# Kernel tuning notes

Hardware: AMD Instinct MI355X
Metric: run time of the kernel (lower is better)

## Reference

```python
import jax, jax.numpy as jnp
import numpy as np

V, E, H, LE, B, T = 32001, 512, 512, 512, 128, 512
EPS = 1e-5


def setup_inputs() -> dict:
    key = jax.random.key(0)
    ks = jax.random.split(key, 12)
    s = 0.02
    return {
        "label": jax.random.randint(ks[0], (B, T), 0, V, dtype=jnp.int64) if jax.config.jax_enable_x64 else jax.random.randint(ks[0], (B, T), 0, V, dtype=jnp.int32),
        "label_len": jax.random.randint(ks[1], (B,), 0, T, dtype=jnp.int32),
        "embed_w": jax.random.normal(ks[2], (V, E), jnp.float32) * s,
        "i2h_w": jax.random.normal(ks[3], (5 * H, E), jnp.float32) * s,
        "i2h_b": jax.random.normal(ks[4], (5 * H,), jnp.float32) * s,
        "h2h_w": jax.random.normal(ks[5], (5 * H, H), jnp.float32) * s,
        "h2h_b": jax.random.normal(ks[6], (5 * H,), jnp.float32) * s,
        "lin0_w": jax.random.normal(ks[7], (LE, H), jnp.float32) * s,
        "lin0_b": jax.random.normal(ks[8], (LE,), jnp.float32) * s,
        "bn0_g": jnp.ones((LE,), jnp.float32),
        "bn0_b": jnp.zeros((LE,), jnp.float32),
        "lin1_w": jax.random.normal(ks[9], (LE, LE), jnp.float32) * s,
        "lin1_b": jax.random.normal(ks[10], (LE,), jnp.float32) * s,
        "bn1_g": jnp.ones((LE,), jnp.float32),
        "bn1_b": jnp.zeros((LE,), jnp.float32),
    }


def _batchnorm(x, g, b):
    # BatchNorm1d in training mode: biased batch statistics over batch dim
    m = jnp.mean(x, axis=0)
    v = jnp.mean((x - m) ** 2, axis=0)
    return (x - m) * jax.lax.rsqrt(v + EPS) * g + b


def reference(label, label_len, embed_w, i2h_w, i2h_b, h2h_w, h2h_b,
              lin0_w, lin0_b, bn0_g, bn0_b, lin1_w, lin1_b, bn1_g, bn1_b):
    xt = embed_w[label]                                   # [B,T,E]
    pre = jnp.einsum('bte,ge->btg', xt, i2h_w) + i2h_b    # precomputed i2h, [B,T,5H]
    pre = pre.transpose(1, 0, 2)                          # [T,B,5H]

    def step(carry, p_t):
        h, c = carry
        s = p_t + h @ h2h_w.T + h2h_b                     # [B,5H]
        sig = jax.nn.sigmoid(s[:, :3 * H])
        in_g, f_g, out_g = sig[:, :H], sig[:, H:2 * H], sig[:, 2 * H:3 * H]
        in_t = jnp.maximum(s[:, 3 * H:4 * H], s[:, 4 * H:5 * H])  # maxout transform
        nc = f_g * c + in_g * in_t
        nh = out_g * jnp.tanh(nc)
        return (nh, nc), nh

    h0 = jnp.zeros((B, H), pre.dtype)
    _, outs = jax.lax.scan(step, (h0, h0), pre)           # outs: [T,B,H]

    # pick output at timestep label_len[i] for each sample
    x = outs[label_len, jnp.arange(B)]                    # [B,H]

    x = _batchnorm(x @ lin0_w.T + lin0_b, bn0_g, bn0_b)
    x = jax.nn.relu(x)                                    # dropout identity (eval)
    x = _batchnorm(x @ lin1_w.T + lin1_b, bn1_g, bn1_b)
    return x
```

## Files before the change

### kernel.cpp

```cpp
#include <hip/hip_runtime.h>

typedef _Float16 h16x8 __attribute__((ext_vector_type(8)));
typedef _Float16 h16x4 __attribute__((ext_vector_type(4)));
typedef float fx4 __attribute__((ext_vector_type(4)));
typedef unsigned int u32x4 __attribute__((ext_vector_type(4)));
typedef unsigned long long ull;

#define PRE_S 2560.0f
#define PRE_INV (1.0f / 2560.0f)

__global__ __launch_bounds__(256) void f2h_kernel(const float* __restrict__ src,
                                                  _Float16* __restrict__ dst,
                                                  int n4) {
  int i = blockIdx.x * 256 + threadIdx.x;
  if (i < n4) {
    float4 v = ((const float4*)src)[i];
    h16x4 o = {(_Float16)v.x, (_Float16)v.y, (_Float16)v.z, (_Float16)v.w};
    *(h16x4*)&dst[i * 4] = o;
  }
}

__global__ __launch_bounds__(256) void gemm1_kernel(
    const int* __restrict__ label, const int* __restrict__ label_len,
    const float* __restrict__ embed_w,
    const _Float16* __restrict__ Bh,
    signed char* __restrict__ pre8) {
  const int bx = blockIdx.x;
  const int by = blockIdx.y;
  const int bidx = by >> 2;
  const int t0 = (by & 3) * 128;
  if (t0 > label_len[bidx]) return;

  const int tid = threadIdx.x;
  const int lane = tid & 63;
  const int wv = tid >> 6;
  const int wm = (wv & 1) * 64;
  const int wn = (wv >> 1) * 64;

  __shared__ _Float16 As[128 * 40];
  __shared__ _Float16 Bs[128 * 40];

  fx4 zero = {0.f, 0.f, 0.f, 0.f};
  fx4 acc[4][4];
  for (int a = 0; a < 4; a++)
    for (int b = 0; b < 4; b++) acc[a][b] = zero;

#pragma unroll 1
  for (int k0 = 0; k0 < 512; k0 += 32) {
#pragma unroll
    for (int q = 0; q < 2; q++) {
      int chunk = tid + q * 256;
      int row = chunk >> 2;
      int ko = (chunk & 3) * 8;
      int arow = label[bidx * 512 + t0 + row];
      const float* ap = &embed_w[(size_t)arow * 512 + k0 + ko];
      float4 a0 = *(const float4*)ap;
      float4 a1 = *(const float4*)(ap + 4);
      h16x8 av = {(_Float16)a0.x, (_Float16)a0.y, (_Float16)a0.z, (_Float16)a0.w,
                  (_Float16)a1.x, (_Float16)a1.y, (_Float16)a1.z, (_Float16)a1.w};
      h16x8 bv = *(const h16x8*)&Bh[(size_t)(bx * 128 + row) * 512 + k0 + ko];
      *(h16x8*)&As[row * 40 + ko] = av;
      *(h16x8*)&Bs[row * 40 + ko] = bv;
    }
    __syncthreads();
    h16x8 af[4], bfr[4];
#pragma unroll
    for (int i = 0; i < 4; i++) {
      af[i]  = *(const h16x8*)&As[(wm + i * 16 + (lane & 15)) * 40 + (lane >> 4) * 8];
      bfr[i] = *(const h16x8*)&Bs[(wn + i * 16 + (lane & 15)) * 40 + (lane >> 4) * 8];
    }
#pragma unroll
    for (int mi = 0; mi < 4; mi++)
#pragma unroll
      for (int ni = 0; ni < 4; ni++)
        acc[mi][ni] = __builtin_amdgcn_mfma_f32_16x16x32_f16(af[mi], bfr[ni], acc[mi][ni], 0, 0, 0);
    __syncthreads();
  }

#pragma unroll
  for (int mi = 0; mi < 4; mi++)
#pragma unroll
    for (int ni = 0; ni < 4; ni++)
#pragma unroll
      for (int r = 0; r < 4; r++) {
        int rowm = wm + mi * 16 + (lane >> 4) * 4 + r;
        int t = t0 + rowm;
        int n = bx * 128 + wn + ni * 16 + (lane & 15);
        float v = acc[mi][ni][r] * PRE_S;
        int q = (int)rintf(v);
        q = q > 127 ? 127 : (q < -127 ? -127 : q);
        int g = n >> 9, ju = n & 511, j = ju >> 3, u = ju & 7;
        pre8[(((size_t)t * 64 + j) * 128 + bidx) * 40 + g * 8 + u] = (signed char)q;
      }
}

#define NWG 128
__global__ __launch_bounds__(256, 1) void lstm_kernel(
    const int* __restrict__ label_len,
    const float* __restrict__ h2h_w,
    const float* __restrict__ h2h_b,
    const float* __restrict__ i2h_b,
    const signed char* __restrict__ pre8,
    _Float16* __restrict__ hfrag,
    float* __restrict__ xsel,
    int* __restrict__ flags) {
  const int j   = blockIdx.x >> 1;
  const int bh  = blockIdx.x & 1;
  const int tid = threadIdx.x;
  const int lane = tid & 63;
  const int wv = tid >> 6;

  __shared__ _Float16 Wl[3 * 16 * 64 * 8];
  __shared__ _Float16 s_s[64 * 48];
  __shared__ int ll_s[64];

  for (int slot = tid; slot < 3 * 16 * 64; slot += 256) {
    int nt = slot / (16 * 64);
    int rem = slot - nt * (16 * 64);
    int kt = rem >> 6;
    int l = rem & 63;
    int p = nt * 16 + (l & 15);
    int k0 = kt * 32 + (l >> 4) * 8;
    h16x8 tv;
    if (p < 40) {
      int r = (p >> 3) * 512 + j * 8 + (p & 7);
      const float* src = h2h_w + (size_t)r * 512 + k0;
#pragma unroll
      for (int q = 0; q < 8; q++) tv[q] = (_Float16)src[q];
    } else {
#pragma unroll
      for (int q = 0; q < 8; q++) tv[q] = (_Float16)0.f;
    }
    *(h16x8*)&Wl[slot * 8] = tv;
  }
  if (tid < 64) ll_s[tid] = label_len[bh * 64 + tid];

  const int ue = (tid & 3) * 2;
  const int bp = tid >> 2;
  float bias_r[2][5];
#pragma unroll
  for (int uu = 0; uu < 2; uu++)
#pragma unroll
    for (int g = 0; g < 5; g++)
      bias_r[uu][g] = h2h_b[g * 512 + j * 8 + ue + uu] + i2h_b[g * 512 + j * 8 + ue + uu];

  const int pbb = (bh * 4 + (bp >> 4)) * 16 + (j >> 2);
  const int plc = (bp & 15) | ((j & 3) << 4);
  unsigned int* pdst0 = (unsigned int*)(hfrag + (size_t)pbb * 512 + plc * 8 + ue);
  unsigned int* pdst1 = (unsigned int*)(hfrag + 65536 + (size_t)pbb * 512 + plc * 8 + ue);

  float c_reg[2] = {0.f, 0.f};
  __syncthreads();

#pragma unroll 1
  for (int t = 0; t < 512; ++t) {
    unsigned short pr[5];
    {
      const signed char* pt = pre8 + (((size_t)t * 64 + j) * 128 + bh * 64) * 40;
#pragma unroll
      for (int g = 0; g < 5; g++)
        pr[g] = *(const unsigned short*)&pt[bp * 40 + g * 8 + ue];
    }

    if (t > 0) {
      if (wv == 0) {
        const int* fp = flags + (bh * 64 + lane) * 32;
        while (true) {
          int v = __hip_atomic_load(fp, __ATOMIC_RELAXED, __HIP_MEMORY_SCOPE_AGENT);
          if (__ballot(v >= t) == 0xFFFFFFFFFFFFFFFFull) break;
          __builtin_amdgcn_s_sleep(1);
        }
      }
      __syncthreads();

      const _Float16* hpb = hfrag + ((t - 1) & 1) * 65536
                          + (size_t)((bh * 4 + wv) * 16) * 512 + lane * 8;
      u32x4 areg[16];
#pragma unroll
      for (int kt = 0; kt < 16; ++kt) {
        const void* ap = (const void*)(hpb + kt * 512);
        asm volatile("global_load_dwordx4 %0, %1, off sc0 sc1"
                     : "=v"(areg[kt]) : "v"(ap) : "memory");
      }
      asm volatile("s_waitcnt vmcnt(0)" ::: "memory");

      fx4 zero = {0.f, 0.f, 0.f, 0.f};
      fx4 acc[3] = {zero, zero, zero};
#pragma unroll
      for (int kt = 0; kt < 16; ++kt) {
        union { u32x4 u; h16x8 v; } a;
        a.u = areg[kt];
#pragma unroll
        for (int nt = 0; nt < 3; nt++) {
          h16x8 bfr = *(const h16x8*)&Wl[((nt * 16 + kt) * 64 + lane) * 8];
          acc[nt] = __builtin_amdgcn_mfma_f32_16x16x32_f16(a.v, bfr, acc[nt], 0, 0, 0);
        }
      }
#pragma unroll
      for (int nt = 0; nt < 3; nt++)
#pragma unroll
        for (int r = 0; r < 4; r++) {
          int b = wv * 16 + (lane >> 4) * 4 + r;
          s_s[b * 48 + nt * 16 + (lane & 15)] = (_Float16)acc[nt][r];
        }
      __syncthreads();
    }

    float nh2[2];
#pragma unroll
    for (int uu = 0; uu < 2; uu++) {
      float sv[5];
#pragma unroll
      for (int g = 0; g < 5; g++) {
        signed char qb = (signed char)(uu == 0 ? (pr[g] & 0xFF) : (pr[g] >> 8));
        float base = (t > 0) ? (float)s_s[bp * 48 + g * 8 + ue + uu] : 0.f;
        sv[g] = base + (float)qb * PRE_INV + bias_r[uu][g];
      }
      float ing = 1.f / (1.f + __expf(-sv[0]));
      float fg  = 1.f / (1.f + __expf(-sv[1]));
      float og  = 1.f / (1.f + __expf(-sv[2]));
      float itv = fmaxf(sv[3], sv[4]);
      float nc = fg * c_reg[uu] + ing * itv;
      c_reg[uu] = nc;
      nh2[uu] = og * tanhf(nc);
    }
    {
      union { _Float16 h[2]; unsigned int u; } pk;
      pk.h[0] = (_Float16)nh2[0];
      pk.h[1] = (_Float16)nh2[1];
      __hip_atomic_store((t & 1) ? pdst1 : pdst0, pk.u,
                         __ATOMIC_RELAXED, __HIP_MEMORY_SCOPE_AGENT);
      if (ll_s[bp] == t) {
        union { float f[2]; ull u; } xk;
        xk.f[0] = nh2[0];
        xk.f[1] = nh2[1];
        __hip_atomic_store((ull*)&xsel[(bh * 64 + bp) * 512 + j * 8 + ue], xk.u,
                           __ATOMIC_RELAXED, __HIP_MEMORY_SCOPE_AGENT);
      }
    }

    asm volatile("s_waitcnt vmcnt(0)" ::: "memory");
    __syncthreads();
    if (tid == 0)
      __hip_atomic_store(flags + (bh * 64 + j) * 32, t + 1,
                         __ATOMIC_RELAXED, __HIP_MEMORY_SCOPE_AGENT);
  }
}

__global__ __launch_bounds__(256) void fgemm_kernel(
    const float* __restrict__ X, const float* __restrict__ W,
    const float* __restrict__ bias, float* __restrict__ Y) {
  const int n0 = blockIdx.x * 64;
  const int m0 = blockIdx.y * 64;
  const int tid = threadIdx.x;
  const int tx = tid & 15, ty = tid >> 4;

  __shared__ float Xs[64 * 68];
  __shared__ float Wt[64 * 68];

  float acc[4][4] = {};
#pragma unroll 1
  for (int k0 = 0; k0 < 512; k0 += 64) {
#pragma unroll
    for (int q = 0; q < 4; q++) {
      int id = tid + q * 256;
      int r = id >> 4, c = id & 15;
      float4 xv = *(const float4*)&X[(m0 + r) * 512 + k0 + c * 4];
      *(float4*)&Xs[r * 68 + c * 4] = xv;
      float4 wvv = *(const float4*)&W[(n0 + r) * 512 + k0 + c * 4];
      Wt[(c * 4 + 0) * 68 + r] = wvv.x;
      Wt[(c * 4 + 1) * 68 + r] = wvv.y;
      Wt[(c * 4 + 2) * 68 + r] = wvv.z;
      Wt[(c * 4 + 3) * 68 + r] = wvv.w;
    }
    __syncthreads();
#pragma unroll 4
    for (int kk = 0; kk < 64; kk++) {
      float a[4], b[4];
#pragma unroll
      for (int i = 0; i < 4; i++) a[i] = Xs[(ty * 4 + i) * 68 + kk];
#pragma unroll
      for (int jj = 0; jj < 4; jj++) b[jj] = Wt[kk * 68 + tx * 4 + jj];
#pragma unroll
      for (int i = 0; i < 4; i++)
#pragma unroll
        for (int jj = 0; jj < 4; jj++) acc[i][jj] += a[i] * b[jj];
    }
    __syncthreads();
  }
#pragma unroll
  for (int i = 0; i < 4; i++)
#pragma unroll
    for (int jj = 0; jj < 4; jj++) {
      int n = n0 + tx * 4 + jj;
      Y[(m0 + ty * 4 + i) * 512 + n] = acc[i][jj] + bias[n];
    }
}

__global__ __launch_bounds__(256) void bn_kernel(float* __restrict__ Y,
    const float* __restrict__ gam, const float* __restrict__ bet, int relu) {
  const int cx = threadIdx.x & 15;
  const int rg = threadIdx.x >> 4;
  const int col = blockIdx.x * 16 + cx;
  __shared__ float rs[16 * 17], rs2[16 * 17];
  float s = 0.f, s2 = 0.f;
#pragma unroll
  for (int i = 0; i < 8; i++) {
    float v = Y[(rg * 8 + i) * 512 + col];
    s += v; s2 += v * v;
  }
  rs[rg * 17 + cx] = s;
  rs2[rg * 17 + cx] = s2;
  __syncthreads();
  if (threadIdx.x < 16) {
    float S = 0.f, S2 = 0.f;
#pragma unroll
    for (int q = 0; q < 16; q++) { S += rs[q * 17 + threadIdx.x]; S2 += rs2[q * 17 + threadIdx.x]; }
    float mean = S / 128.f;
    float var = S2 / 128.f - mean * mean;
    rs[threadIdx.x] = mean;
    rs2[threadIdx.x] = rsqrtf(var + 1e-5f);
  }
  __syncthreads();
  float mean = rs[cx], rstd = rs2[cx];
  float gv = gam[col], bv = bet[col];
#pragma unroll
  for (int i = 0; i < 8; i++) {
    int idx = (rg * 8 + i) * 512 + col;
    float v = (Y[idx] - mean) * rstd * gv + bv;
    if (relu) v = fmaxf(v, 0.f);
    Y[idx] = v;
  }
}

extern "C" void kernel_launch(void* const* d_in, const int* in_sizes, int n_in,
                              void* d_out, int out_size, void* d_ws, size_t ws_size,
                              hipStream_t stream) {
  const int* label      = (const int*)d_in[0];
  const int* label_len  = (const int*)d_in[1];
  const float* embed_w  = (const float*)d_in[2];
  const float* i2h_w    = (const float*)d_in[3];
  const float* i2h_b    = (const float*)d_in[4];
  const float* h2h_w    = (const float*)d_in[5];
  const float* h2h_b    = (const float*)d_in[6];
  const float* lin0_w   = (const float*)d_in[7];
  const float* lin0_b   = (const float*)d_in[8];
  const float* bn0_g    = (const float*)d_in[9];
  const float* bn0_b    = (const float*)d_in[10];
  const float* lin1_w   = (const float*)d_in[11];
  const float* lin1_b   = (const float*)d_in[12];
  const float* bn1_g    = (const float*)d_in[13];
  const float* bn1_b    = (const float*)d_in[14];
  float* out = (float*)d_out;
  char* ws = (char*)d_ws;

  const size_t OFF_FLAGS = 0;
  const size_t OFF_I2H  = 16384;
  const size_t OFF_PRE  = OFF_I2H + (size_t)2560 * 512 * 2;
  const size_t OFF_H    = OFF_PRE + (size_t)512 * 128 * 2560;
  const size_t OFF_XSEL = OFF_H + (size_t)2 * 128 * 512 * 2;
  const size_t OFF_Y0   = OFF_XSEL + (size_t)128 * 512 * 4;

  int* flags = (int*)(ws + OFF_FLAGS);
  _Float16* i2h_h = (_Float16*)(ws + OFF_I2H);
  signed char* pre8 = (signed char*)(ws + OFF_PRE);
  _Float16* hfrag = (_Float16*)(ws + OFF_H);
  float* xsel = (float*)(ws + OFF_XSEL);
  float* y0   = (float*)(ws + OFF_Y0);

  hipMemsetAsync(ws + OFF_FLAGS, 0, 16384, stream);

  {
    int n4 = (2560 * 512) / 4;
    f2h_kernel<<<(n4 + 255) / 256, 256, 0, stream>>>(i2h_w, i2h_h, n4);
  }
  gemm1_kernel<<<dim3(20, 512), 256, 0, stream>>>(label, label_len, embed_w, i2h_h, pre8);
  lstm_kernel<<<dim3(NWG), 256, 0, stream>>>(label_len, h2h_w, h2h_b, i2h_b, pre8, hfrag, xsel, flags);
  fgemm_kernel<<<dim3(8, 2), 256, 0, stream>>>(xsel, lin0_w, lin0_b, y0);
  bn_kernel<<<dim3(32), 256, 0, stream>>>(y0, bn0_g, bn0_b, 1);
  fgemm_kernel<<<dim3(8, 2), 256, 0, stream>>>(y0, lin1_w, lin1_b, out);
  bn_kernel<<<dim3(32), 256, 0, stream>>>(out, bn1_g, bn1_b, 0);
}
```

Baseline: 2.491 ms.

## Replace flag-based grid sync with sentinel-poisoned per-timestep hidden buffers

Drops the per-step flag publish and wait, along with their vmcnt drain and extra barriers. Each timestep's hidden state now goes to its own slot in a large buffer that is pre-filled with 0xFF. Consumers keep reloading their fragments until no 0xFFFFFFFF sentinel remains, so the data itself is the readiness signal. This removes a round trip of flag latency on each of the 512 serial steps. The cost is a 64MB memset per call, a double-buffered LDS s_s, and reliance on 32-bit stores landing atomically and on a real fp16 pair never encoding as 0xFFFFFFFF (a NaN pattern).

Result: slower. 2.812 ms (+12.9%).

```diff
diff --git a/kernel.cpp b/kernel.cpp
--- a/kernel.cpp
+++ b/kernel.cpp
@@ -102,8 +102,7 @@
     const float* __restrict__ i2h_b,
     const signed char* __restrict__ pre8,
     _Float16* __restrict__ hfrag,
-    float* __restrict__ xsel,
-    int* __restrict__ flags) {
+    float* __restrict__ xsel) {
   const int j   = blockIdx.x >> 1;
   const int bh  = blockIdx.x & 1;
   const int tid = threadIdx.x;
@@ -111,7 +110,7 @@
   const int wv = tid >> 6;
 
   __shared__ _Float16 Wl[3 * 16 * 64 * 8];
-  __shared__ _Float16 s_s[64 * 48];
+  __shared__ _Float16 s_s[2][64 * 48];
   __shared__ int ll_s[64];
 
   for (int slot = tid; slot < 3 * 16 * 64; slot += 256) {
@@ -146,8 +145,7 @@
 
   const int pbb = (bh * 4 + (bp >> 4)) * 16 + (j >> 2);
   const int plc = (bp & 15) | ((j & 3) << 4);
-  unsigned int* pdst0 = (unsigned int*)(hfrag + (size_t)pbb * 512 + plc * 8 + ue);
-  unsigned int* pdst1 = (unsigned int*)(hfrag + 65536 + (size_t)pbb * 512 + plc * 8 + ue);
+  const size_t poff = (size_t)pbb * 512 + plc * 8 + ue;
 
   float c_reg[2] = {0.f, 0.f};
   __syncthreads();
@@ -163,26 +161,26 @@
     }
 
     if (t > 0) {
-      if (wv == 0) {
-        const int* fp = flags + (bh * 64 + lane) * 32;
-        while (true) {
-          int v = __hip_atomic_load(fp, __ATOMIC_RELAXED, __HIP_MEMORY_SCOPE_AGENT);
-          if (__ballot(v >= t) == 0xFFFFFFFFFFFFFFFFull) break;
-          __builtin_amdgcn_s_sleep(1);
-        }
-      }
-      __syncthreads();
-
-      const _Float16* hpb = hfrag + ((t - 1) & 1) * 65536
+      const _Float16* hpb = hfrag + (size_t)(t - 1) * 65536
                           + (size_t)((bh * 4 + wv) * 16) * 512 + lane * 8;
       u32x4 areg[16];
-#pragma unroll
-      for (int kt = 0; kt < 16; ++kt) {
-        const void* ap = (const void*)(hpb + kt * 512);
-        asm volatile("global_load_dwordx4 %0, %1, off sc0 sc1"
-                     : "=v"(areg[kt]) : "v"(ap) : "memory");
-      }
-      asm volatile("s_waitcnt vmcnt(0)" ::: "memory");
+      while (true) {
+#pragma unroll
+        for (int kt = 0; kt < 16; ++kt) {
+          const void* ap = (const void*)(hpb + kt * 512);
+          asm volatile("global_load_dwordx4 %0, %1, off sc0 sc1"
+                       : "=v"(areg[kt]) : "v"(ap) : "memory");
+        }
+        asm volatile("s_waitcnt vmcnt(0)" ::: "memory");
+        unsigned bad = 0;
+#pragma unroll
+        for (int kt = 0; kt < 16; ++kt)
+#pragma unroll
+          for (int q = 0; q < 4; q++)
+            bad |= (areg[kt][q] == 0xFFFFFFFFu) ? 1u : 0u;
+        if (__ballot(bad != 0) == 0) break;
+        __builtin_amdgcn_s_sleep(1);
+      }
 
       fx4 zero = {0.f, 0.f, 0.f, 0.f};
       fx4 acc[3] = {zero, zero, zero};
@@ -201,7 +199,7 @@
 #pragma unroll
         for (int r = 0; r < 4; r++) {
           int b = wv * 16 + (lane >> 4) * 4 + r;
-          s_s[b * 48 + nt * 16 + (lane & 15)] = (_Float16)acc[nt][r];
+          s_s[t & 1][b * 48 + nt * 16 + (lane & 15)] = (_Float16)acc[nt][r];
         }
       __syncthreads();
     }
@@ -213,7 +211,7 @@
 #pragma unroll
       for (int g = 0; g < 5; g++) {
         signed char qb = (signed char)(uu == 0 ? (pr[g] & 0xFF) : (pr[g] >> 8));
-        float base = (t > 0) ? (float)s_s[bp * 48 + g * 8 + ue + uu] : 0.f;
+        float base = (t > 0) ? (float)s_s[t & 1][bp * 48 + g * 8 + ue + uu] : 0.f;
         sv[g] = base + (float)qb * PRE_INV + bias_r[uu][g];
       }
       float ing = 1.f / (1.f + __expf(-sv[0]));
@@ -228,7 +226,7 @@
       union { _Float16 h[2]; unsigned int u; } pk;
       pk.h[0] = (_Float16)nh2[0];
       pk.h[1] = (_Float16)nh2[1];
-      __hip_atomic_store((t & 1) ? pdst1 : pdst0, pk.u,
+      __hip_atomic_store((unsigned int*)(hfrag + (size_t)t * 65536 + poff), pk.u,
                          __ATOMIC_RELAXED, __HIP_MEMORY_SCOPE_AGENT);
       if (ll_s[bp] == t) {
         union { float f[2]; ull u; } xk;
@@ -238,12 +236,6 @@
                            __ATOMIC_RELAXED, __HIP_MEMORY_SCOPE_AGENT);
       }
     }
-
-    asm volatile("s_waitcnt vmcnt(0)" ::: "memory");
-    __syncthreads();
-    if (tid == 0)
-      __hip_atomic_store(flags + (bh * 64 + j) * 32, t + 1,
-                         __ATOMIC_RELAXED, __HIP_MEMORY_SCOPE_AGENT);
   }
 }
 
@@ -354,28 +346,27 @@
   float* out = (float*)d_out;
   char* ws = (char*)d_ws;
 
-  const size_t OFF_FLAGS = 0;
-  const size_t OFF_I2H  = 16384;
+  const size_t OFF_I2H  = 0;
   const size_t OFF_PRE  = OFF_I2H + (size_t)2560 * 512 * 2;
-  const size_t OFF_H    = OFF_PRE + (size_t)512 * 128 * 2560;
-  const size_t OFF_XSEL = OFF_H + (size_t)2 * 128 * 512 * 2;
+  const size_t OFF_HF   = OFF_PRE + (size_t)512 * 128 * 2560;
+  const size_t HF_BYTES = (size_t)512 * 128 * 512 * 2;
+  const size_t OFF_XSEL = OFF_HF + HF_BYTES;
   const size_t OFF_Y0   = OFF_XSEL + (size_t)128 * 512 * 4;
 
-  int* flags = (int*)(ws + OFF_FLAGS);
   _Float16* i2h_h = (_Float16*)(ws + OFF_I2H);
   signed char* pre8 = (signed char*)(ws + OFF_PRE);
-  _Float16* hfrag = (_Float16*)(ws + OFF_H);
+  _Float16* hfrag = (_Float16*)(ws + OFF_HF);
   float* xsel = (float*)(ws + OFF_XSEL);
   float* y0   = (float*)(ws + OFF_Y0);
 
-  hipMemsetAsync(ws + OFF_FLAGS, 0, 16384, stream);
+  hipMemsetAsync(ws + OFF_HF, 0xFF, HF_BYTES, stream);
 
   {
     int n4 = (2560 * 512) / 4;
     f2h_kernel<<<(n4 + 255) / 256, 256, 0, stream>>>(i2h_w, i2h_h, n4);
   }
   gemm1_kernel<<<dim3(20, 512), 256, 0, stream>>>(label, label_len, embed_w, i2h_h, pre8);
-  lstm_kernel<<<dim3(NWG), 256, 0, stream>>>(label_len, h2h_w, h2h_b, i2h_b, pre8, hfrag, xsel, flags);
+  lstm_kernel<<<dim3(NWG), 256, 0, stream>>>(label_len, h2h_w, h2h_b, i2h_b, pre8, hfrag, xsel);
   fgemm_kernel<<<dim3(8, 2), 256, 0, stream>>>(xsel, lin0_w, lin0_b, y0);
   bn_kernel<<<dim3(32), 256, 0, stream>>>(y0, bn0_g, bn0_b, 1);
   fgemm_kernel<<<dim3(8, 2), 256, 0, stream>>>(y0, lin1_w, lin1_b, out);
```
